# Kernel optimization log

Hardware: AMD Instinct MI355X
Metric: run time of the kernel (lower is better)

Reference implementation:

```python
import jax, jax.numpy as jnp
import numpy as np

IN_Q, OUT_Q = 32, 32
GRID_H, GRID_W = 64, 64
FREQ_H, FREQ_W = GRID_H, GRID_W // 2 + 1
BATCH = 32
INIT_SCALE = 0.02


def setup_inputs() -> dict:
    key = jax.random.key(0)
    keys = jax.random.split(key, 9)
    inp = {"x": jax.random.normal(keys[0], (BATCH, 4 * IN_Q, GRID_H, GRID_W), dtype=jnp.float32)}
    names = ["kr_w", "kr_x", "kr_y", "kr_z", "ki_w", "ki_x", "ki_y", "ki_z"]
    for i, n in enumerate(names):
        inp[n] = jax.random.normal(keys[i + 1], (IN_Q, OUT_Q, FREQ_H, FREQ_W), dtype=jnp.float32) * INIT_SCALE
    return inp


def reference(x, kr_w, kr_x, kr_y, kr_z, ki_w, ki_x, ki_y, ki_z):
    q = IN_Q
    # Split quaternion components and FFT each: [B, q, H, Wf] complex
    xs = jnp.stack([x[:, :q], x[:, q:2 * q], x[:, 2 * q:3 * q], x[:, 3 * q:]])  # [4,B,q,H,W]
    Xs = jnp.fft.rfft2(xs, s=(GRID_H, GRID_W), axes=(-2, -1))  # [4,B,q,H,Wf]
    # Complex kernels, stacked: [4, in_q, out_q, H, Wf]
    Ws = jnp.stack([kr_w + 1j * ki_w, kr_x + 1j * ki_x, kr_y + 1j * ki_y, kr_z + 1j * ki_z])
    # All 16 pairwise contractions in one einsum: C[p,q] = W_p contracted with X_q
    C = jnp.einsum('piohw,qbihw->pqbohw', Ws, Xs)  # [4,4,B,out,H,Wf]
    # Hamilton product combination
    Pw = C[0, 0] - C[1, 1] - C[2, 2] - C[3, 3]
    Px = C[0, 1] + C[1, 0] + C[2, 3] - C[3, 2]
    Py = C[0, 2] - C[1, 3] + C[2, 0] + C[3, 1]
    Pz = C[0, 3] + C[1, 2] - C[2, 1] + C[3, 0]
    P = jnp.stack([Pw, Px, Py, Pz])  # [4,B,out,H,Wf]
    o = jnp.fft.irfft2(P, s=(GRID_H, GRID_W), axes=(-2, -1))  # [4,B,out,H,W]
    # cat along channel dim: [B, 4*out, H, W]
    return jnp.concatenate([o[0], o[1], o[2], o[3]], axis=1)
```

## Files before the change

kernel.cpp:

```cpp
#include <hip/hip_runtime.h>

#define FH 64
#define FW 64
#define NWF 33
#define NBIN (FH*NWF)
#define NIMG 4096
#define PI2 6.283185307179586f

typedef unsigned short u16;
typedef unsigned int u32;
typedef __attribute__((ext_vector_type(8))) short bf16x8;
typedef __attribute__((ext_vector_type(8))) _Float16 f16x8;
typedef __attribute__((ext_vector_type(4))) unsigned short u16x4;
typedef __attribute__((ext_vector_type(4))) float f32x4;
typedef __attribute__((ext_vector_type(4))) int   i32x4;

__device__ __forceinline__ u16 f2bf(float f) {
    unsigned u = __float_as_uint(f);
    unsigned r = (u + 0x7FFFu + ((u >> 16) & 1u)) >> 16;
    return (u16)r;
}
__device__ __forceinline__ u16 f2h(float f) {
    _Float16 h = (_Float16)f;
    return __builtin_bit_cast(u16, h);
}
__device__ __forceinline__ float2 upk(u32 v) {
    return make_float2(__uint_as_float(v << 16), __uint_as_float(v & 0xFFFF0000u));
}
__device__ __forceinline__ u32 pk(float2 v) {
    return (u32)f2bf(v.x) | ((u32)f2bf(v.y) << 16);
}
__device__ __forceinline__ f16x8 negh(f16x8 v) {
    i32x4 t = __builtin_bit_cast(i32x4, v);
    t ^= (int)0x80008000;
    return __builtin_bit_cast(f16x8, t);
}

__global__ __launch_bounds__(512, 4) void fft_fwd_kernel(const float* __restrict__ x,
                                                         u32* __restrict__ Xs)
{
    __shared__ __align__(16) u16 mats[2][64*72];
    __shared__ __align__(16) u16 wbuf[4][6912];

    const int tid  = threadIdx.x;
    const int lane = tid & 63;
    const int wid  = tid >> 6;
    const int slot = wid >> 1;
    const int half = wid & 1;
    const int ltid = (half << 6) | lane;
    const int a16  = lane & 15;
    const int q    = lane >> 4;

    const int img = blockIdx.x * 4 + slot;
    const int qc = img >> 10;
    const int b  = (img >> 5) & 31;
    const int ci = img & 31;
    const float* __restrict__ src = x + ((size_t)b*128 + (size_t)qc*32 + ci) * (FH*FW);

    for (int t = tid; t < 4096; t += 512) {
        int a = t >> 6, bb = t & 63;
        float sn, cs;
        __sincosf(PI2 * (float)((a*bb) & 63) * (1.f/64.f), &sn, &cs);
        mats[0][a*72 + bb] = f2h(cs);
        mats[1][a*72 + bb] = f2h(sn);
    }
    u16* xb = wbuf[slot];
    for (int i = 0; i < 8; ++i) {
        int idx4 = i*128 + ltid;
        float4 v = ((const float4*)src)[idx4];
        int h = idx4 >> 4, c4 = (idx4 & 15) * 4;
        u16x4 hv = { f2h(v.x), f2h(v.y), f2h(v.z), f2h(v.w) };
        *(u16x4*)&xb[h*64 + c4] = hv;
    }
    __syncthreads();

    f16x8 xf[2][2];
    #pragma unroll
    for (int mtl = 0; mtl < 2; ++mtl)
        #pragma unroll
        for (int ks = 0; ks < 2; ++ks)
            xf[mtl][ks] = *(const f16x8*)&xb[(16*(2*half + mtl) + a16)*64 + ks*32 + q*8];
    __syncthreads();

    u16* ST = wbuf[slot];
    #pragma unroll
    for (int mtl = 0; mtl < 2; ++mtl) {
        const int mt = 2*half + mtl;
        f32x4 are[3], aim[3];
        #pragma unroll
        for (int nt = 0; nt < 3; ++nt) { are[nt] = (f32x4){0,0,0,0}; aim[nt] = (f32x4){0,0,0,0}; }
        #pragma unroll
        for (int nt = 0; nt < 3; ++nt)
            #pragma unroll
            for (int ks = 0; ks < 2; ++ks) {
                const int rb = (16*nt + a16)*72 + ks*32 + q*8;
                f16x8 cf = *(const f16x8*)&mats[0][rb];
                f16x8 sf = *(const f16x8*)&mats[1][rb];
                are[nt] = __builtin_amdgcn_mfma_f32_16x16x32_f16(xf[mtl][ks], cf, are[nt], 0, 0, 0);
                aim[nt] = __builtin_amdgcn_mfma_f32_16x16x32_f16(xf[mtl][ks], negh(sf), aim[nt], 0, 0, 0);
            }
        const int hb = 16*mt + 4*q;
        #pragma unroll
        for (int nt = 0; nt < 3; ++nt) {
            u16x4 re4 = { f2h(are[nt][0]), f2h(are[nt][1]), f2h(are[nt][2]), f2h(are[nt][3]) };
            u16x4 im4 = { f2h(aim[nt][0]), f2h(aim[nt][1]), f2h(aim[nt][2]), f2h(aim[nt][3]) };
            *(u16x4*)&ST[(16*nt + a16)*72 + hb]        = re4;
            *(u16x4*)&ST[(48 + 16*nt + a16)*72 + hb]   = im4;
        }
    }
    __syncthreads();

    f16x8 bfr[2][3][2];
    #pragma unroll
    for (int ri = 0; ri < 2; ++ri)
        #pragma unroll
        for (int nt = 0; nt < 3; ++nt)
            #pragma unroll
            for (int ks = 0; ks < 2; ++ks)
                bfr[ri][nt][ks] = *(const f16x8*)&ST[(ri*48 + 16*nt + a16)*72 + ks*32 + q*8];
    __syncthreads();

    u32* sbin = (u32*)wbuf[slot];
    #pragma unroll
    for (int mtl = 0; mtl < 2; ++mtl) {
        const int mt = 2*half + mtl;
        f16x8 cfa[2], sfa[2], nsf[2];
        #pragma unroll
        for (int ks = 0; ks < 2; ++ks) {
            const int rb = (16*mt + a16)*72 + ks*32 + q*8;
            cfa[ks] = *(const f16x8*)&mats[0][rb];
            sfa[ks] = *(const f16x8*)&mats[1][rb];
            nsf[ks] = negh(sfa[ks]);
        }
        #pragma unroll
        for (int nt = 0; nt < 3; ++nt) {
            f32x4 xre = (f32x4){0,0,0,0}, xim = (f32x4){0,0,0,0};
            #pragma unroll
            for (int ks = 0; ks < 2; ++ks) {
                xre = __builtin_amdgcn_mfma_f32_16x16x32_f16(cfa[ks], bfr[0][nt][ks], xre, 0, 0, 0);
                xre = __builtin_amdgcn_mfma_f32_16x16x32_f16(sfa[ks], bfr[1][nt][ks], xre, 0, 0, 0);
                xim = __builtin_amdgcn_mfma_f32_16x16x32_f16(cfa[ks], bfr[1][nt][ks], xim, 0, 0, 0);
                xim = __builtin_amdgcn_mfma_f32_16x16x32_f16(nsf[ks], bfr[0][nt][ks], xim, 0, 0, 0);
            }
            const int k = 16*nt + a16;
            if (k < 33) {
                #pragma unroll
                for (int r = 0; r < 4; ++r)
                    sbin[(16*mt + 4*q + r)*34 + k] = pk(make_float2(xre[r], xim[r]));
            }
        }
    }
    __syncthreads();

    u32* __restrict__ dst = Xs + (size_t)img * NBIN;
    for (int i = 0; i < 17; ++i) {
        int t = i*128 + ltid;
        if (t < NBIN) {
            int hf = t / 33;
            dst[t] = sbin[hf*34 + (t - hf*33)];
        }
    }
}

__global__ __launch_bounds__(256) void xpose_x_kernel(const u32* __restrict__ Xs,
                                                      u32* __restrict__ XT)
{
    const int g    = blockIdx.x;
    const int bin0 = blockIdx.y * 32;
    __shared__ u32 tile[32][33];
    const int tid = threadIdx.x;
    #pragma unroll
    for (int it = 0; it < 4; ++it) {
        int e = tid + it*256;
        int imgL = e >> 5, binL = e & 31;
        tile[imgL][binL] = Xs[(size_t)(g*32 + imgL) * NBIN + bin0 + binL];
    }
    __syncthreads();
    const int q = g >> 5, b = g & 31;
    #pragma unroll
    for (int it = 0; it < 2; ++it) {
        int e = tid + it*256;
        int binL = e >> 4, pr = e & 15;
        u32 v0 = tile[pr*2][binL], v1 = tile[pr*2 + 1][binL];
        u32 re = (v0 & 0xFFFFu) | (v1 << 16);
        u32 im = (v0 >> 16) | (v1 & 0xFFFF0000u);
        size_t base = ((size_t)(bin0 + binL)*8 + q*2) * 512 + b*16 + pr;
        XT[base]       = re;
        XT[base + 512] = im;
    }
}

__global__ __launch_bounds__(256) void prep_w_kernel(
    const float* __restrict__ s0, const float* __restrict__ s1,
    const float* __restrict__ s2, const float* __restrict__ s3,
    const float* __restrict__ s4, const float* __restrict__ s5,
    const float* __restrict__ s6, const float* __restrict__ s7,
    u16* __restrict__ WT)
{
    const int bt = blockIdx.x;
    const int a  = blockIdx.y >> 2;
    const int o0 = (blockIdx.y & 3) * 8;
    const float* __restrict__ src =
        (a==0)?s0:(a==1)?s1:(a==2)?s2:(a==3)?s3:(a==4)?s4:(a==5)?s5:(a==6)?s6:s7;
    const int bin0 = bt * 32;
    __shared__ u16 lds2[32*264];
    const int tid = threadIdx.x;

    #pragma unroll
    for (int it = 0; it < 8; ++it) {
        int e = tid + it*256;
        int f4 = e & 7, rt = e >> 3;
        int i = rt & 31, oo = rt >> 5;
        int io = i*32 + o0 + oo;
        float4 v = ((const float4*)src)[(size_t)io*(NBIN/4) + bt*8 + f4];
        int chL = oo*32 + i;
        int bb = f4*4;
        lds2[(bb+0)*264 + chL] = f2bf(v.x);
        lds2[(bb+1)*264 + chL] = f2bf(v.y);
        lds2[(bb+2)*264 + chL] = f2bf(v.z);
        lds2[(bb+3)*264 + chL] = f2bf(v.w);
    }
    __syncthreads();
    const int p = a & 3, ri = a >> 2;
    #pragma unroll
    for (int it = 0; it < 4; ++it) {
        int e = tid + it*256;
        int binL = e >> 5, c8 = e & 31;
        bf16x8 v = *(const bf16x8*)&lds2[binL*264 + c8*8];
        size_t d = ((size_t)(bin0 + binL)*8 + p*2 + ri)*1024 + o0*32 + c8*8;
        *(bf16x8*)(WT + d) = v;
    }
}

__global__ __launch_bounds__(256) void contract_kernel(
    const u16* __restrict__ XT, const u16* __restrict__ WT,
    u32* __restrict__ P)
{
    const int bid  = blockIdx.x;
    const int bin  = (bid & 7) * (NBIN/8) + (bid >> 3);
    const int wid  = threadIdx.x >> 6;
    const int lane = threadIdx.x & 63;
    const int bh = wid >> 1, oh = wid & 1;
    const int row = lane & 15, kg = lane >> 4;

    const u16* __restrict__ xb = XT + (size_t)bin * 8192;
    const u16* __restrict__ wb = WT + (size_t)bin * 8192;

    bf16x8 ax[4][2];
    #pragma unroll
    for (int q = 0; q < 4; ++q)
        #pragma unroll
        for (int ri = 0; ri < 2; ++ri)
            ax[q][ri] = *(const bf16x8*)(xb + ((q*2 + ri)*32 + bh*16 + row)*32 + kg*8);

    bf16x8 wpos[4][2], wneg[4][2];
    #pragma unroll
    for (int p = 0; p < 4; ++p)
        #pragma unroll
        for (int ri = 0; ri < 2; ++ri) {
            bf16x8 w = *(const bf16x8*)(wb + ((p*2 + ri)*32 + oh*16 + row)*32 + kg*8);
            wpos[p][ri] = w;
            i32x4 t = __builtin_bit_cast(i32x4, w);
            t ^= (int)0x80008000;
            wneg[p][ri] = __builtin_bit_cast(bf16x8, t);
        }

    f32x4 acc[4][2];
    #pragma unroll
    for (int c = 0; c < 4; ++c)
        #pragma unroll
        for (int ri = 0; ri < 2; ++ri)
            acc[c][ri] = (f32x4){0.f, 0.f, 0.f, 0.f};

    constexpr int PI_[4][4] = {{0,1,2,3},{1,0,3,2},{2,3,0,1},{3,2,1,0}};
    constexpr int SG_[4][4] = {{1,-1,-1,-1},{1,1,-1,1},{1,1,1,-1},{1,-1,1,1}};
    #pragma unroll
    for (int c = 0; c < 4; ++c)
        #pragma unroll
        for (int q = 0; q < 4; ++q) {
            const int  p   = PI_[c][q];
            const bool pos = SG_[c][q] > 0;
            bf16x8 wr_s = pos ? wpos[p][0] : wneg[p][0];
            bf16x8 wi_s = pos ? wpos[p][1] : wneg[p][1];
            bf16x8 wi_m = pos ? wneg[p][1] : wpos[p][1];
            acc[c][0] = __builtin_amdgcn_mfma_f32_16x16x32_bf16(ax[q][0], wr_s, acc[c][0], 0, 0, 0);
            acc[c][0] = __builtin_amdgcn_mfma_f32_16x16x32_bf16(ax[q][1], wi_m, acc[c][0], 0, 0, 0);
            acc[c][1] = __builtin_amdgcn_mfma_f32_16x16x32_bf16(ax[q][1], wr_s, acc[c][1], 0, 0, 0);
            acc[c][1] = __builtin_amdgcn_mfma_f32_16x16x32_bf16(ax[q][0], wi_s, acc[c][1], 0, 0, 0);
        }

    u32* __restrict__ dst = P + (size_t)bin * 4096;
    #pragma unroll
    for (int c = 0; c < 4; ++c)
        #pragma unroll
        for (int r = 0; r < 4; ++r) {
            int b_ = bh*16 + kg*4 + r;
            int o  = oh*16 + row;
            dst[c*1024 + b_*32 + o] = pk(make_float2(acc[c][0][r], acc[c][1][r]));
        }
}

__global__ __launch_bounds__(256) void pxpose_kernel(const u32* __restrict__ P,
                                                     u32* __restrict__ PT)
{
    const int bin0 = blockIdx.x * 32;
    const int img0 = blockIdx.y * 32;
    __shared__ u32 tile[32][33];
    const int tid = threadIdx.x;
    #pragma unroll
    for (int it = 0; it < 4; ++it) {
        int e = tid + it*256;
        int bi = e >> 5, im = e & 31;
        tile[bi][im] = P[(size_t)(bin0 + bi) * 4096 + img0 + im];
    }
    __syncthreads();
    #pragma unroll
    for (int it = 0; it < 4; ++it) {
        int e = tid + it*256;
        int im = e >> 5, bi = e & 31;
        PT[(size_t)(img0 + im) * NBIN + bin0 + bi] = tile[bi][im];
    }
}

__global__ __launch_bounds__(512, 4) void fft_inv_kernel(const u32* __restrict__ PT,
                                                         float* __restrict__ out)
{
    __shared__ __align__(16) u16 mats[2][64*72];
    __shared__ __align__(16) u16 wbuf[4][7168];

    const int tid  = threadIdx.x;
    const int lane = tid & 63;
    const int wid  = tid >> 6;
    const int slot = wid >> 1;
    const int half = wid & 1;
    const int ltid = (half << 6) | lane;
    const int a16  = lane & 15;
    const int q    = lane >> 4;

    const int img = blockIdx.x * 4 + slot;
    const int c  = img >> 10;
    const int b  = (img >> 5) & 31;
    const int oc = img & 31;

    for (int t = tid; t < 4096; t += 512) {
        int a = t >> 6, bb = t & 63;
        float sn, cs;
        __sincosf(PI2 * (float)((a*bb) & 63) * (1.f/64.f), &sn, &cs);
        mats[0][a*72 + bb] = f2h(cs);
        mats[1][a*72 + bb] = f2h(sn);
    }

    u16* ETre = wbuf[slot];
    u16* ETim = wbuf[slot] + 48*72;
    for (int j = 33*72 + ltid; j < 48*72; j += 128) {
        ETre[j] = 0;
        ETim[j] = 0;
    }
    const u32* __restrict__ srcP = PT + (size_t)img * NBIN;
    for (int i = 0; i < 17; ++i) {
        int t = i*128 + ltid;
        if (t < NBIN) {
            int hf = t / 33, k = t - hf*33;
            float2 v = upk(srcP[t]);
            ETre[k*72 + hf] = f2h(v.x);
            ETim[k*72 + hf] = f2h(v.y);
        }
    }
    __syncthreads();

    f16x8 ere[2][2], eim[2][2];
    #pragma unroll
    for (int mtl = 0; mtl < 2; ++mtl) {
        const int mt = 2*half + mtl;
        if (mt < 3) {
            #pragma unroll
            for (int ks = 0; ks < 2; ++ks) {
                ere[mtl][ks] = *(const f16x8*)&ETre[(16*mt + a16)*72 + ks*32 + q*8];
                eim[mtl][ks] = *(const f16x8*)&ETim[(16*mt + a16)*72 + ks*32 + q*8];
            }
        }
    }
    __syncthreads();

    u16* Tre = wbuf[slot];
    u16* Tim = wbuf[slot] + 64*56;
    #pragma unroll
    for (int mtl = 0; mtl < 2; ++mtl) {
        const int mt = 2*half + mtl;
        if (mt < 3) {
            #pragma unroll
            for (int nt = 0; nt < 4; ++nt) {
                f32x4 tre = (f32x4){0,0,0,0}, tim = (f32x4){0,0,0,0};
                #pragma unroll
                for (int ks = 0; ks < 2; ++ks) {
                    const int rb = (16*nt + a16)*72 + ks*32 + q*8;
                    f16x8 cf = *(const f16x8*)&mats[0][rb];
                    f16x8 sf = *(const f16x8*)&mats[1][rb];
                    tre = __builtin_amdgcn_mfma_f32_16x16x32_f16(ere[mtl][ks], cf, tre, 0, 0, 0);
                    tre = __builtin_amdgcn_mfma_f32_16x16x32_f16(eim[mtl][ks], negh(sf), tre, 0, 0, 0);
                    tim = __builtin_amdgcn_mfma_f32_16x16x32_f16(ere[mtl][ks], sf, tim, 0, 0, 0);
                    tim = __builtin_amdgcn_mfma_f32_16x16x32_f16(eim[mtl][ks], cf, tim, 0, 0, 0);
                }
                const int m0 = 16*mt + 4*q;
                u16x4 r4, i4;
                #pragma unroll
                for (int r = 0; r < 4; ++r) {
                    int m = m0 + r;
                    float s = (m == 0 || m == 32) ? (1.f/4096.f) : (2.f/4096.f);
                    r4[r] = (m < 33) ? f2h(tre[r] * s) : (u16)0;
                    i4[r] = (m < 33) ? f2h(tim[r] * s) : (u16)0;
                }
                *(u16x4*)&Tre[(16*nt + a16)*56 + m0] = r4;
                *(u16x4*)&Tim[(16*nt + a16)*56 + m0] = i4;
            }
        }
    }
    __syncthreads();

    float* __restrict__ dst = out + ((size_t)b*128 + (size_t)c*32 + oc) * (FH*FW);
    #pragma unroll
    for (int mtl = 0; mtl < 2; ++mtl) {
        const int mt = 2*half + mtl;
        f16x8 tfr[2], tfi[2];
        #pragma unroll
        for (int ks = 0; ks < 2; ++ks) {
            const int mbase = ks*32 + q*8;
            if (mbase < 48) {
                tfr[ks] = *(const f16x8*)&Tre[(16*mt + a16)*56 + mbase];
                tfi[ks] = *(const f16x8*)&Tim[(16*mt + a16)*56 + mbase];
            } else {
                tfr[ks] = (f16x8){0,0,0,0,0,0,0,0};
                tfi[ks] = (f16x8){0,0,0,0,0,0,0,0};
            }
        }
        #pragma unroll
        for (int nt = 0; nt < 4; ++nt) {
            f32x4 acc = (f32x4){0,0,0,0};
            #pragma unroll
            for (int ks = 0; ks < 2; ++ks) {
                const int rb = (16*nt + a16)*72 + ks*32 + q*8;
                f16x8 cf = *(const f16x8*)&mats[0][rb];
                f16x8 sf = *(const f16x8*)&mats[1][rb];
                acc = __builtin_amdgcn_mfma_f32_16x16x32_f16(tfr[ks], cf, acc, 0, 0, 0);
                acc = __builtin_amdgcn_mfma_f32_16x16x32_f16(tfi[ks], negh(sf), acc, 0, 0, 0);
            }
            #pragma unroll
            for (int r = 0; r < 4; ++r)
                dst[(16*mt + 4*q + r)*64 + 16*nt + a16] = acc[r];
        }
    }
}

extern "C" void kernel_launch(void* const* d_in, const int* in_sizes, int n_in,
                              void* d_out, int out_size, void* d_ws, size_t ws_size,
                              hipStream_t stream)
{
    const float* x   = (const float*)d_in[0];
    const float* krw = (const float*)d_in[1];
    const float* krx = (const float*)d_in[2];
    const float* kry = (const float*)d_in[3];
    const float* krz = (const float*)d_in[4];
    const float* kiw = (const float*)d_in[5];
    const float* kix = (const float*)d_in[6];
    const float* kiy = (const float*)d_in[7];
    const float* kiz = (const float*)d_in[8];

    const size_t R = (size_t)NBIN * 8192 * sizeof(u16);
    u16* XT = (u16*)d_ws;
    u32* PT = (u32*)d_ws;
    u16* WT = (u16*)((char*)d_ws + R);
    u32* Xs = (u32*)((char*)d_ws + 2*R);
    u32* P  = Xs;
    float* out = (float*)d_out;

    prep_w_kernel<<<dim3(66, 32), 256, 0, stream>>>(krw, krx, kry, krz,
                                                    kiw, kix, kiy, kiz, WT);
    fft_fwd_kernel<<<dim3(NIMG/4), 512, 0, stream>>>(x, Xs);
    xpose_x_kernel<<<dim3(128, NBIN/32), 256, 0, stream>>>(Xs, (u32*)XT);
    contract_kernel<<<dim3(NBIN), 256, 0, stream>>>(XT, WT, P);
    pxpose_kernel<<<dim3(NBIN/32, NIMG/32), 256, 0, stream>>>(P, PT);
    fft_inv_kernel<<<dim3(NIMG/4), 512, 0, stream>>>(PT, out);
}
```

Baseline: 119.8 us.

## Merge weight prep into forward FFT launch and load input directly to registers

Combines the weight-transpose kernel and the forward FFT into one launch, with block index selecting the role, which removes a launch and lets the two independent stages overlap on the GPU. The FFT path now loads its input from global memory straight into MFMA fragments, skipping the LDS staging. It also writes spectra directly to global memory instead of packing them through LDS first. Risks include uncoalesced global stores, uncoalesced input loads, and the weight-prep blocks using 512 threads with a larger shared footprint, which may lower occupancy.

```diff
diff --git a/kernel.cpp b/kernel.cpp
--- a/kernel.cpp
+++ b/kernel.cpp
@@ -36,128 +36,156 @@
     return __builtin_bit_cast(f16x8, t);
 }
 
-__global__ __launch_bounds__(512, 4) void fft_fwd_kernel(const float* __restrict__ x,
-                                                         u32* __restrict__ Xs)
-{
-    __shared__ __align__(16) u16 mats[2][64*72];
-    __shared__ __align__(16) u16 wbuf[4][6912];
-
-    const int tid  = threadIdx.x;
-    const int lane = tid & 63;
-    const int wid  = tid >> 6;
-    const int slot = wid >> 1;
-    const int half = wid & 1;
-    const int ltid = (half << 6) | lane;
-    const int a16  = lane & 15;
-    const int q    = lane >> 4;
-
-    const int img = blockIdx.x * 4 + slot;
-    const int qc = img >> 10;
-    const int b  = (img >> 5) & 31;
-    const int ci = img & 31;
-    const float* __restrict__ src = x + ((size_t)b*128 + (size_t)qc*32 + ci) * (FH*FW);
-
-    for (int t = tid; t < 4096; t += 512) {
-        int a = t >> 6, bb = t & 63;
-        float sn, cs;
-        __sincosf(PI2 * (float)((a*bb) & 63) * (1.f/64.f), &sn, &cs);
-        mats[0][a*72 + bb] = f2h(cs);
-        mats[1][a*72 + bb] = f2h(sn);
-    }
-    u16* xb = wbuf[slot];
-    for (int i = 0; i < 8; ++i) {
-        int idx4 = i*128 + ltid;
-        float4 v = ((const float4*)src)[idx4];
-        int h = idx4 >> 4, c4 = (idx4 & 15) * 4;
-        u16x4 hv = { f2h(v.x), f2h(v.y), f2h(v.z), f2h(v.w) };
-        *(u16x4*)&xb[h*64 + c4] = hv;
-    }
-    __syncthreads();
-
-    f16x8 xf[2][2];
-    #pragma unroll
-    for (int mtl = 0; mtl < 2; ++mtl)
-        #pragma unroll
-        for (int ks = 0; ks < 2; ++ks)
-            xf[mtl][ks] = *(const f16x8*)&xb[(16*(2*half + mtl) + a16)*64 + ks*32 + q*8];
-    __syncthreads();
-
-    u16* ST = wbuf[slot];
-    #pragma unroll
-    for (int mtl = 0; mtl < 2; ++mtl) {
-        const int mt = 2*half + mtl;
-        f32x4 are[3], aim[3];
-        #pragma unroll
-        for (int nt = 0; nt < 3; ++nt) { are[nt] = (f32x4){0,0,0,0}; aim[nt] = (f32x4){0,0,0,0}; }
-        #pragma unroll
-        for (int nt = 0; nt < 3; ++nt)
+__global__ __launch_bounds__(512, 4) void fwd_prep_kernel(
+    const float* __restrict__ x, u32* __restrict__ Xs,
+    const float* __restrict__ s0, const float* __restrict__ s1,
+    const float* __restrict__ s2, const float* __restrict__ s3,
+    const float* __restrict__ s4, const float* __restrict__ s5,
+    const float* __restrict__ s6, const float* __restrict__ s7,
+    u16* __restrict__ WT)
+{
+    __shared__ __align__(16) u16 sm[36864];
+    const int tid = threadIdx.x;
+
+    if (blockIdx.x < 1024) {
+        const int lane = tid & 63;
+        const int wid  = tid >> 6;
+        const int slot = wid >> 1;
+        const int half = wid & 1;
+        const int a16  = lane & 15;
+        const int q    = lane >> 4;
+
+        const int img = blockIdx.x * 4 + slot;
+        const int qc = img >> 10;
+        const int b  = (img >> 5) & 31;
+        const int ci = img & 31;
+        const float* __restrict__ src = x + ((size_t)b*128 + (size_t)qc*32 + ci) * (FH*FW);
+
+        u16* mats0 = sm;
+        u16* mats1 = sm + 64*72;
+        u16* ST    = sm + 9216 + slot*6912;
+
+        for (int t = tid; t < 4096; t += 512) {
+            int a = t >> 6, bb = t & 63;
+            float sn, cs;
+            __sincosf(PI2 * (float)((a*bb) & 63) * (1.f/64.f), &sn, &cs);
+            mats0[a*72 + bb] = f2h(cs);
+            mats1[a*72 + bb] = f2h(sn);
+        }
+
+        f16x8 xf[2][2];
+        #pragma unroll
+        for (int mtl = 0; mtl < 2; ++mtl)
             #pragma unroll
             for (int ks = 0; ks < 2; ++ks) {
-                const int rb = (16*nt + a16)*72 + ks*32 + q*8;
-                f16x8 cf = *(const f16x8*)&mats[0][rb];
-                f16x8 sf = *(const f16x8*)&mats[1][rb];
-                are[nt] = __builtin_amdgcn_mfma_f32_16x16x32_f16(xf[mtl][ks], cf, are[nt], 0, 0, 0);
-                aim[nt] = __builtin_amdgcn_mfma_f32_16x16x32_f16(xf[mtl][ks], negh(sf), aim[nt], 0, 0, 0);
-            }
-        const int hb = 16*mt + 4*q;
-        #pragma unroll
-        for (int nt = 0; nt < 3; ++nt) {
-            u16x4 re4 = { f2h(are[nt][0]), f2h(are[nt][1]), f2h(are[nt][2]), f2h(are[nt][3]) };
-            u16x4 im4 = { f2h(aim[nt][0]), f2h(aim[nt][1]), f2h(aim[nt][2]), f2h(aim[nt][3]) };
-            *(u16x4*)&ST[(16*nt + a16)*72 + hb]        = re4;
-            *(u16x4*)&ST[(48 + 16*nt + a16)*72 + hb]   = im4;
-        }
-    }
-    __syncthreads();
-
-    f16x8 bfr[2][3][2];
-    #pragma unroll
-    for (int ri = 0; ri < 2; ++ri)
-        #pragma unroll
-        for (int nt = 0; nt < 3; ++nt)
-            #pragma unroll
-            for (int ks = 0; ks < 2; ++ks)
-                bfr[ri][nt][ks] = *(const f16x8*)&ST[(ri*48 + 16*nt + a16)*72 + ks*32 + q*8];
-    __syncthreads();
-
-    u32* sbin = (u32*)wbuf[slot];
-    #pragma unroll
-    for (int mtl = 0; mtl < 2; ++mtl) {
-        const int mt = 2*half + mtl;
-        f16x8 cfa[2], sfa[2], nsf[2];
-        #pragma unroll
-        for (int ks = 0; ks < 2; ++ks) {
-            const int rb = (16*mt + a16)*72 + ks*32 + q*8;
-            cfa[ks] = *(const f16x8*)&mats[0][rb];
-            sfa[ks] = *(const f16x8*)&mats[1][rb];
-            nsf[ks] = negh(sfa[ks]);
-        }
-        #pragma unroll
-        for (int nt = 0; nt < 3; ++nt) {
-            f32x4 xre = (f32x4){0,0,0,0}, xim = (f32x4){0,0,0,0};
+                const float* rp = src + (16*(2*half + mtl) + a16)*64 + ks*32 + q*8;
+                float4 v0 = *(const float4*)rp;
+                float4 v1 = *(const float4*)(rp + 4);
+                xf[mtl][ks] = (f16x8){ (_Float16)v0.x, (_Float16)v0.y, (_Float16)v0.z, (_Float16)v0.w,
+                                       (_Float16)v1.x, (_Float16)v1.y, (_Float16)v1.z, (_Float16)v1.w };
+            }
+        __syncthreads();
+
+        #pragma unroll
+        for (int mtl = 0; mtl < 2; ++mtl) {
+            const int mt = 2*half + mtl;
+            f32x4 are[3], aim[3];
+            #pragma unroll
+            for (int nt = 0; nt < 3; ++nt) { are[nt] = (f32x4){0,0,0,0}; aim[nt] = (f32x4){0,0,0,0}; }
+            #pragma unroll
+            for (int nt = 0; nt < 3; ++nt)
+                #pragma unroll
+                for (int ks = 0; ks < 2; ++ks) {
+                    const int rb = (16*nt + a16)*72 + ks*32 + q*8;
+                    f16x8 cf = *(const f16x8*)&mats0[rb];
+                    f16x8 sf = *(const f16x8*)&mats1[rb];
+                    are[nt] = __builtin_amdgcn_mfma_f32_16x16x32_f16(xf[mtl][ks], cf, are[nt], 0, 0, 0);
+                    aim[nt] = __builtin_amdgcn_mfma_f32_16x16x32_f16(xf[mtl][ks], negh(sf), aim[nt], 0, 0, 0);
+                }
+            const int hb = 16*mt + 4*q;
+            #pragma unroll
+            for (int nt = 0; nt < 3; ++nt) {
+                u16x4 re4 = { f2h(are[nt][0]), f2h(are[nt][1]), f2h(are[nt][2]), f2h(are[nt][3]) };
+                u16x4 im4 = { f2h(aim[nt][0]), f2h(aim[nt][1]), f2h(aim[nt][2]), f2h(aim[nt][3]) };
+                *(u16x4*)&ST[(16*nt + a16)*72 + hb]      = re4;
+                *(u16x4*)&ST[(48 + 16*nt + a16)*72 + hb] = im4;
+            }
+        }
+        __syncthreads();
+
+        f16x8 bfr[2][3][2];
+        #pragma unroll
+        for (int ri = 0; ri < 2; ++ri)
+            #pragma unroll
+            for (int nt = 0; nt < 3; ++nt)
+                #pragma unroll
+                for (int ks = 0; ks < 2; ++ks)
+                    bfr[ri][nt][ks] = *(const f16x8*)&ST[(ri*48 + 16*nt + a16)*72 + ks*32 + q*8];
+
+        u32* __restrict__ dst = Xs + (size_t)img * NBIN;
+        #pragma unroll
+        for (int mtl = 0; mtl < 2; ++mtl) {
+            const int mt = 2*half + mtl;
+            f16x8 cfa[2], sfa[2], nsf[2];
             #pragma unroll
             for (int ks = 0; ks < 2; ++ks) {
-                xre = __builtin_amdgcn_mfma_f32_16x16x32_f16(cfa[ks], bfr[0][nt][ks], xre, 0, 0, 0);
-                xre = __builtin_amdgcn_mfma_f32_16x16x32_f16(sfa[ks], bfr[1][nt][ks], xre, 0, 0, 0);
-                xim = __builtin_amdgcn_mfma_f32_16x16x32_f16(cfa[ks], bfr[1][nt][ks], xim, 0, 0, 0);
-                xim = __builtin_amdgcn_mfma_f32_16x16x32_f16(nsf[ks], bfr[0][nt][ks], xim, 0, 0, 0);
-            }
-            const int k = 16*nt + a16;
-            if (k < 33) {
+                const int rb = (16*mt + a16)*72 + ks*32 + q*8;
+                cfa[ks] = *(const f16x8*)&mats0[rb];
+                sfa[ks] = *(const f16x8*)&mats1[rb];
+                nsf[ks] = negh(sfa[ks]);
+            }
+            #pragma unroll
+            for (int nt = 0; nt < 3; ++nt) {
+                f32x4 xre = (f32x4){0,0,0,0}, xim = (f32x4){0,0,0,0};
                 #pragma unroll
-                for (int r = 0; r < 4; ++r)
-                    sbin[(16*mt + 4*q + r)*34 + k] = pk(make_float2(xre[r], xim[r]));
-            }
-        }
-    }
-    __syncthreads();
-
-    u32* __restrict__ dst = Xs + (size_t)img * NBIN;
-    for (int i = 0; i < 17; ++i) {
-        int t = i*128 + ltid;
-        if (t < NBIN) {
-            int hf = t / 33;
-            dst[t] = sbin[hf*34 + (t - hf*33)];
+                for (int ks = 0; ks < 2; ++ks) {
+                    xre = __builtin_amdgcn_mfma_f32_16x16x32_f16(cfa[ks], bfr[0][nt][ks], xre, 0, 0, 0);
+                    xre = __builtin_amdgcn_mfma_f32_16x16x32_f16(sfa[ks], bfr[1][nt][ks], xre, 0, 0, 0);
+                    xim = __builtin_amdgcn_mfma_f32_16x16x32_f16(cfa[ks], bfr[1][nt][ks], xim, 0, 0, 0);
+                    xim = __builtin_amdgcn_mfma_f32_16x16x32_f16(nsf[ks], bfr[0][nt][ks], xim, 0, 0, 0);
+                }
+                const int k = 16*nt + a16;
+                if (k < 33) {
+                    #pragma unroll
+                    for (int r = 0; r < 4; ++r)
+                        dst[(16*mt + 4*q + r)*33 + k] = pk(make_float2(xre[r], xim[r]));
+                }
+            }
+        }
+    } else {
+        const int pb = blockIdx.x - 1024;
+        const int bt = pb % 66;
+        const int ay = pb / 66;
+        const int a  = ay >> 2;
+        const int o0 = (ay & 3) * 8;
+        const float* __restrict__ src =
+            (a==0)?s0:(a==1)?s1:(a==2)?s2:(a==3)?s3:(a==4)?s4:(a==5)?s5:(a==6)?s6:s7;
+        const int bin0 = bt * 32;
+        u16* lds2 = sm;
+
+        #pragma unroll
+        for (int it = 0; it < 4; ++it) {
+            int e = tid + it*512;
+            int f4 = e & 7, rt = e >> 3;
+            int i = rt & 31, oo = rt >> 5;
+            int io = i*32 + o0 + oo;
+            float4 v = ((const float4*)src)[(size_t)io*(NBIN/4) + bt*8 + f4];
+            int chL = oo*32 + i;
+            int bb = f4*4;
+            lds2[(bb+0)*264 + chL] = f2bf(v.x);
+            lds2[(bb+1)*264 + chL] = f2bf(v.y);
+            lds2[(bb+2)*264 + chL] = f2bf(v.z);
+            lds2[(bb+3)*264 + chL] = f2bf(v.w);
+        }
+        __syncthreads();
+        const int p = a & 3, ri = a >> 2;
+        #pragma unroll
+        for (int it = 0; it < 2; ++it) {
+            int e = tid + it*512;
+            int binL = e >> 5, c8 = e & 31;
+            bf16x8 v = *(const bf16x8*)&lds2[binL*264 + c8*8];
+            size_t d = ((size_t)(bin0 + binL)*8 + p*2 + ri)*1024 + o0*32 + c8*8;
+            *(bf16x8*)(WT + d) = v;
         }
     }
 }
@@ -187,48 +215,6 @@
         size_t base = ((size_t)(bin0 + binL)*8 + q*2) * 512 + b*16 + pr;
         XT[base]       = re;
         XT[base + 512] = im;
-    }
-}
-
-__global__ __launch_bounds__(256) void prep_w_kernel(
-    const float* __restrict__ s0, const float* __restrict__ s1,
-    const float* __restrict__ s2, const float* __restrict__ s3,
-    const float* __restrict__ s4, const float* __restrict__ s5,
-    const float* __restrict__ s6, const float* __restrict__ s7,
-    u16* __restrict__ WT)
-{
-    const int bt = blockIdx.x;
-    const int a  = blockIdx.y >> 2;
-    const int o0 = (blockIdx.y & 3) * 8;
-    const float* __restrict__ src =
-        (a==0)?s0:(a==1)?s1:(a==2)?s2:(a==3)?s3:(a==4)?s4:(a==5)?s5:(a==6)?s6:s7;
-    const int bin0 = bt * 32;
-    __shared__ u16 lds2[32*264];
-    const int tid = threadIdx.x;
-
-    #pragma unroll
-    for (int it = 0; it < 8; ++it) {
-        int e = tid + it*256;
-        int f4 = e & 7, rt = e >> 3;
-        int i = rt & 31, oo = rt >> 5;
-        int io = i*32 + o0 + oo;
-        float4 v = ((const float4*)src)[(size_t)io*(NBIN/4) + bt*8 + f4];
-        int chL = oo*32 + i;
-        int bb = f4*4;
-        lds2[(bb+0)*264 + chL] = f2bf(v.x);
-        lds2[(bb+1)*264 + chL] = f2bf(v.y);
-        lds2[(bb+2)*264 + chL] = f2bf(v.z);
-        lds2[(bb+3)*264 + chL] = f2bf(v.w);
-    }
-    __syncthreads();
-    const int p = a & 3, ri = a >> 2;
-    #pragma unroll
-    for (int it = 0; it < 4; ++it) {
-        int e = tid + it*256;
-        int binL = e >> 5, c8 = e & 31;
-        bf16x8 v = *(const bf16x8*)&lds2[binL*264 + c8*8];
-        size_t d = ((size_t)(bin0 + binL)*8 + p*2 + ri)*1024 + o0*32 + c8*8;
-        *(bf16x8*)(WT + d) = v;
     }
 }
 
@@ -473,9 +459,9 @@
     u32* P  = Xs;
     float* out = (float*)d_out;
 
-    prep_w_kernel<<<dim3(66, 32), 256, 0, stream>>>(krw, krx, kry, krz,
-                                                    kiw, kix, kiy, kiz, WT);
-    fft_fwd_kernel<<<dim3(NIMG/4), 512, 0, stream>>>(x, Xs);
+    fwd_prep_kernel<<<dim3(1024 + 2112), 512, 0, stream>>>(x, Xs,
+                                                           krw, krx, kry, krz,
+                                                           kiw, kix, kiy, kiz, WT);
     xpose_x_kernel<<<dim3(128, NBIN/32), 256, 0, stream>>>(Xs, (u32*)XT);
     contract_kernel<<<dim3(NBIN), 256, 0, stream>>>(XT, WT, P);
     pxpose_kernel<<<dim3(NBIN/32, NIMG/32), 256, 0, stream>>>(P, PT);
```

Measured after the change: 112.6 us. 1.06x faster.

## Restructure forward FFT to one wave per image with register-resident input

Applied to the files above, without the earlier changes.

The forward FFT kernel now assigns one wavefront per image instead of two, with 256 threads per block. Input rows are loaded from global memory straight into f16 MFMA fragments, skipping the shared-memory staging buffer. The intermediate column stage goes through a small per-wave scratch buffer one frequency tile at a time, and results are written directly to global memory without block-wide barriers. Shared memory use and synchronisation both drop, at the cost of uncoalesced strided output stores and a higher per-wave register count.

```diff
diff --git a/kernel.cpp b/kernel.cpp
--- a/kernel.cpp
+++ b/kernel.cpp
@@ -36,128 +36,97 @@
     return __builtin_bit_cast(f16x8, t);
 }
 
-__global__ __launch_bounds__(512, 4) void fft_fwd_kernel(const float* __restrict__ x,
+__global__ __launch_bounds__(256, 4) void fft_fwd_kernel(const float* __restrict__ x,
                                                          u32* __restrict__ Xs)
 {
     __shared__ __align__(16) u16 mats[2][64*72];
-    __shared__ __align__(16) u16 wbuf[4][6912];
+    __shared__ __align__(16) u16 scr[4][2][16*72];
 
     const int tid  = threadIdx.x;
     const int lane = tid & 63;
     const int wid  = tid >> 6;
-    const int slot = wid >> 1;
-    const int half = wid & 1;
-    const int ltid = (half << 6) | lane;
     const int a16  = lane & 15;
-    const int q    = lane >> 4;
-
-    const int img = blockIdx.x * 4 + slot;
-    const int qc = img >> 10;
-    const int b  = (img >> 5) & 31;
-    const int ci = img & 31;
-    const float* __restrict__ src = x + ((size_t)b*128 + (size_t)qc*32 + ci) * (FH*FW);
-
-    for (int t = tid; t < 4096; t += 512) {
+    const int kg   = lane >> 4;
+
+    for (int t = tid; t < 4096; t += 256) {
         int a = t >> 6, bb = t & 63;
         float sn, cs;
         __sincosf(PI2 * (float)((a*bb) & 63) * (1.f/64.f), &sn, &cs);
         mats[0][a*72 + bb] = f2h(cs);
         mats[1][a*72 + bb] = f2h(sn);
     }
-    u16* xb = wbuf[slot];
-    for (int i = 0; i < 8; ++i) {
-        int idx4 = i*128 + ltid;
-        float4 v = ((const float4*)src)[idx4];
-        int h = idx4 >> 4, c4 = (idx4 & 15) * 4;
-        u16x4 hv = { f2h(v.x), f2h(v.y), f2h(v.z), f2h(v.w) };
-        *(u16x4*)&xb[h*64 + c4] = hv;
-    }
-    __syncthreads();
-
-    f16x8 xf[2][2];
-    #pragma unroll
-    for (int mtl = 0; mtl < 2; ++mtl)
-        #pragma unroll
-        for (int ks = 0; ks < 2; ++ks)
-            xf[mtl][ks] = *(const f16x8*)&xb[(16*(2*half + mtl) + a16)*64 + ks*32 + q*8];
-    __syncthreads();
-
-    u16* ST = wbuf[slot];
-    #pragma unroll
-    for (int mtl = 0; mtl < 2; ++mtl) {
-        const int mt = 2*half + mtl;
-        f32x4 are[3], aim[3];
-        #pragma unroll
-        for (int nt = 0; nt < 3; ++nt) { are[nt] = (f32x4){0,0,0,0}; aim[nt] = (f32x4){0,0,0,0}; }
-        #pragma unroll
-        for (int nt = 0; nt < 3; ++nt)
+    __syncthreads();
+
+    const int img = blockIdx.x * 4 + wid;
+    const int qc = img >> 10;
+    const int b  = (img >> 5) & 31;
+    const int ci = img & 31;
+    const float* __restrict__ src = x + ((size_t)b*128 + (size_t)qc*32 + ci) * (FH*FW);
+
+    f16x8 xf[4][2];
+    #pragma unroll
+    for (int mt = 0; mt < 4; ++mt)
+        #pragma unroll
+        for (int ks = 0; ks < 2; ++ks) {
+            const float* rp = src + (16*mt + a16)*64 + ks*32 + kg*8;
+            float4 v0 = *(const float4*)rp;
+            float4 v1 = *(const float4*)(rp + 4);
+            xf[mt][ks] = (f16x8){ (_Float16)v0.x, (_Float16)v0.y, (_Float16)v0.z, (_Float16)v0.w,
+                                  (_Float16)v1.x, (_Float16)v1.y, (_Float16)v1.z, (_Float16)v1.w };
+        }
+
+    u16* sre = scr[wid][0];
+    u16* sim = scr[wid][1];
+    u32* __restrict__ dst = Xs + (size_t)img * NBIN;
+
+    #pragma unroll
+    for (int nt = 0; nt < 3; ++nt) {
+        f32x4 are[4], aim[4];
+        #pragma unroll
+        for (int mt = 0; mt < 4; ++mt) { are[mt] = (f32x4){0,0,0,0}; aim[mt] = (f32x4){0,0,0,0}; }
+        #pragma unroll
+        for (int ks = 0; ks < 2; ++ks) {
+            const int rb = (16*nt + a16)*72 + ks*32 + kg*8;
+            f16x8 cf  = *(const f16x8*)&mats[0][rb];
+            f16x8 nsf = negh(*(const f16x8*)&mats[1][rb]);
+            #pragma unroll
+            for (int mt = 0; mt < 4; ++mt) {
+                are[mt] = __builtin_amdgcn_mfma_f32_16x16x32_f16(xf[mt][ks], cf,  are[mt], 0, 0, 0);
+                aim[mt] = __builtin_amdgcn_mfma_f32_16x16x32_f16(xf[mt][ks], nsf, aim[mt], 0, 0, 0);
+            }
+        }
+        #pragma unroll
+        for (int mt = 0; mt < 4; ++mt) {
+            u16x4 re4 = { f2h(are[mt][0]), f2h(are[mt][1]), f2h(are[mt][2]), f2h(are[mt][3]) };
+            u16x4 im4 = { f2h(aim[mt][0]), f2h(aim[mt][1]), f2h(aim[mt][2]), f2h(aim[mt][3]) };
+            *(u16x4*)&sre[a16*72 + 16*mt + 4*kg] = re4;
+            *(u16x4*)&sim[a16*72 + 16*mt + 4*kg] = im4;
+        }
+        f16x8 br[2], bi[2];
+        #pragma unroll
+        for (int ks = 0; ks < 2; ++ks) {
+            br[ks] = *(const f16x8*)&sre[a16*72 + ks*32 + kg*8];
+            bi[ks] = *(const f16x8*)&sim[a16*72 + ks*32 + kg*8];
+        }
+        const int k = 16*nt + a16;
+        #pragma unroll
+        for (int mt2 = 0; mt2 < 4; ++mt2) {
+            f32x4 xre = (f32x4){0,0,0,0}, xim = (f32x4){0,0,0,0};
             #pragma unroll
             for (int ks = 0; ks < 2; ++ks) {
-                const int rb = (16*nt + a16)*72 + ks*32 + q*8;
+                const int rb = (16*mt2 + a16)*72 + ks*32 + kg*8;
                 f16x8 cf = *(const f16x8*)&mats[0][rb];
                 f16x8 sf = *(const f16x8*)&mats[1][rb];
-                are[nt] = __builtin_amdgcn_mfma_f32_16x16x32_f16(xf[mtl][ks], cf, are[nt], 0, 0, 0);
-                aim[nt] = __builtin_amdgcn_mfma_f32_16x16x32_f16(xf[mtl][ks], negh(sf), aim[nt], 0, 0, 0);
-            }
-        const int hb = 16*mt + 4*q;
-        #pragma unroll
-        for (int nt = 0; nt < 3; ++nt) {
-            u16x4 re4 = { f2h(are[nt][0]), f2h(are[nt][1]), f2h(are[nt][2]), f2h(are[nt][3]) };
-            u16x4 im4 = { f2h(aim[nt][0]), f2h(aim[nt][1]), f2h(aim[nt][2]), f2h(aim[nt][3]) };
-            *(u16x4*)&ST[(16*nt + a16)*72 + hb]        = re4;
-            *(u16x4*)&ST[(48 + 16*nt + a16)*72 + hb]   = im4;
-        }
-    }
-    __syncthreads();
-
-    f16x8 bfr[2][3][2];
-    #pragma unroll
-    for (int ri = 0; ri < 2; ++ri)
-        #pragma unroll
-        for (int nt = 0; nt < 3; ++nt)
-            #pragma unroll
-            for (int ks = 0; ks < 2; ++ks)
-                bfr[ri][nt][ks] = *(const f16x8*)&ST[(ri*48 + 16*nt + a16)*72 + ks*32 + q*8];
-    __syncthreads();
-
-    u32* sbin = (u32*)wbuf[slot];
-    #pragma unroll
-    for (int mtl = 0; mtl < 2; ++mtl) {
-        const int mt = 2*half + mtl;
-        f16x8 cfa[2], sfa[2], nsf[2];
-        #pragma unroll
-        for (int ks = 0; ks < 2; ++ks) {
-            const int rb = (16*mt + a16)*72 + ks*32 + q*8;
-            cfa[ks] = *(const f16x8*)&mats[0][rb];
-            sfa[ks] = *(const f16x8*)&mats[1][rb];
-            nsf[ks] = negh(sfa[ks]);
-        }
-        #pragma unroll
-        for (int nt = 0; nt < 3; ++nt) {
-            f32x4 xre = (f32x4){0,0,0,0}, xim = (f32x4){0,0,0,0};
-            #pragma unroll
-            for (int ks = 0; ks < 2; ++ks) {
-                xre = __builtin_amdgcn_mfma_f32_16x16x32_f16(cfa[ks], bfr[0][nt][ks], xre, 0, 0, 0);
-                xre = __builtin_amdgcn_mfma_f32_16x16x32_f16(sfa[ks], bfr[1][nt][ks], xre, 0, 0, 0);
-                xim = __builtin_amdgcn_mfma_f32_16x16x32_f16(cfa[ks], bfr[1][nt][ks], xim, 0, 0, 0);
-                xim = __builtin_amdgcn_mfma_f32_16x16x32_f16(nsf[ks], bfr[0][nt][ks], xim, 0, 0, 0);
-            }
-            const int k = 16*nt + a16;
+                xre = __builtin_amdgcn_mfma_f32_16x16x32_f16(cf, br[ks], xre, 0, 0, 0);
+                xre = __builtin_amdgcn_mfma_f32_16x16x32_f16(sf, bi[ks], xre, 0, 0, 0);
+                xim = __builtin_amdgcn_mfma_f32_16x16x32_f16(cf, bi[ks], xim, 0, 0, 0);
+                xim = __builtin_amdgcn_mfma_f32_16x16x32_f16(negh(sf), br[ks], xim, 0, 0, 0);
+            }
             if (k < 33) {
                 #pragma unroll
                 for (int r = 0; r < 4; ++r)
-                    sbin[(16*mt + 4*q + r)*34 + k] = pk(make_float2(xre[r], xim[r]));
-            }
-        }
-    }
-    __syncthreads();
-
-    u32* __restrict__ dst = Xs + (size_t)img * NBIN;
-    for (int i = 0; i < 17; ++i) {
-        int t = i*128 + ltid;
-        if (t < NBIN) {
-            int hf = t / 33;
-            dst[t] = sbin[hf*34 + (t - hf*33)];
+                    dst[(16*mt2 + 4*kg + r)*33 + k] = pk(make_float2(xre[r], xim[r]));
+            }
         }
     }
 }
@@ -475,7 +444,7 @@
 
     prep_w_kernel<<<dim3(66, 32), 256, 0, stream>>>(krw, krx, kry, krz,
                                                     kiw, kix, kiy, kiz, WT);
-    fft_fwd_kernel<<<dim3(NIMG/4), 512, 0, stream>>>(x, Xs);
+    fft_fwd_kernel<<<dim3(NIMG/4), 256, 0, stream>>>(x, Xs);
     xpose_x_kernel<<<dim3(128, NBIN/32), 256, 0, stream>>>(Xs, (u32*)XT);
     contract_kernel<<<dim3(NBIN), 256, 0, stream>>>(XT, WT, P);
     pxpose_kernel<<<dim3(NBIN/32, NIMG/32), 256, 0, stream>>>(P, PT);
```

Measured after the change: 123.0 us. 1.03x slower.
